# Performance work log

Hardware: AMD Instinct MI355X
Metric: run time of the kernel (lower is better)

Reference implementation:

```python
import jax, jax.numpy as jnp
import numpy as np

NUM_CLASSES = 21
EPS = 1e-6
MOMENTUM = 0.99
K_WEAK = 16
K_STRONG = 256
PROB_THRESH = 0.95
IGNORE = 255
NEG = -1e30


def _normalize(x, axis=-1):
    # matches F.normalize(p=2) / CosineSimilarity with eps=1e-6
    n = jnp.linalg.norm(x, axis=axis, keepdims=True)
    return x / jnp.maximum(n, EPS)


def setup_inputs() -> dict:
    key = jax.random.key(0)
    k0, k1, k2, k3, k4, k5 = jax.random.split(key, 6)
    B, C, H, W = 8, 256, 128, 128
    feature_weak = jax.random.normal(k0, (B, C, H, W), jnp.float32)
    feature_strong = jax.random.normal(k1, (B, C, H, W), jnp.float32)
    probablity_weak = jax.random.uniform(k2, (B, H, W), jnp.float32)
    memory_bank = jax.random.normal(k3, (NUM_CLASSES, 1, C), jnp.float32)
    pred_weak = jax.random.randint(k4, (B, H, W), 0, NUM_CLASSES)
    ignore_mask = jax.random.randint(k5, (B, H, W), 0, 256)
    return {
        'feature_weak': feature_weak,
        'feature_strong': feature_strong,
        'probablity_weak': probablity_weak,
        'memory_bank': memory_bank,
        'pred_weak': pred_weak,
        'ignore_mask': ignore_mask,
    }


def reference(feature_weak, feature_strong, probablity_weak, memory_bank, pred_weak, ignore_mask):
    B, C, H, W = feature_weak.shape
    N = B * H * W
    fw = feature_weak.transpose(0, 2, 3, 1).reshape(N, C)   # weak pixel feats
    fs = feature_strong.transpose(0, 2, 3, 1).reshape(N, C) # strong pixel feats
    seg = pred_weak.reshape(N)
    ign = ignore_mask.reshape(N)  # same-size bilinear resize (align_corners) is identity
    prob = probablity_weak.reshape(N)

    valid = ign != IGNORE
    conf = valid & (prob > PROB_THRESH)

    cls = jnp.arange(NUM_CLASSES)
    is_cls = seg[None, :] == cls[:, None]        # [K, N]
    m_weak = is_cls & conf[None, :]              # per-class high-confidence mask
    m_strong = is_cls & valid[None, :]
    n_weak = m_weak.sum(axis=1)                  # [K]
    n_strong = m_strong.sum(axis=1)

    protos = memory_bank[:, 0, :]                # [K, C]
    pn = _normalize(protos)
    sim_w = _normalize(fw) @ pn.T                # [N, K] cos(pixel_weak, proto)
    sim_s = _normalize(fs) @ pn.T                # [N, K] cos(pixel_strong, proto)

    sw = jnp.where(m_weak, sim_w.T, NEG)         # [K, N]
    ss = jnp.where(m_strong, -sim_s.T, NEG)      # negate -> bottom-k via top_k
    _, idx_w = jax.lax.top_k(sw, K_WEAK)         # [K, 16] most-similar weak pixels
    _, idx_s = jax.lax.top_k(ss, K_STRONG)       # [K, 256] least-similar strong pixels

    # select_feature duplicates the top element: slots are ranks [0,0,1,...,14]
    ranks = jnp.maximum(jnp.arange(K_WEAK) - 1, 0)
    sel_w = fw[idx_w[:, ranks]]                  # [K, 16, C]
    sel_s = fs[idx_s]                            # [K, 256, C]

    kw = jnp.minimum(K_WEAK, n_weak)
    ks = jnp.minimum(K_STRONG, n_strong)
    valid_w = jnp.arange(K_WEAK)[None, :] < kw[:, None]     # [K, 16]
    valid_s = jnp.arange(K_STRONG)[None, :] < ks[:, None]   # [K, 256]

    # calculate_loss: weak side detached, max over strong dim, sum / strong count
    wn = _normalize(jax.lax.stop_gradient(sel_w))
    sn = _normalize(sel_s)
    cosm = jnp.einsum('kwc,ksc->kws', wn, sn)    # [K, 16, 256]
    cosm = jnp.where(valid_s[:, None, :], cosm, NEG)
    max_sim = jnp.where(valid_w, cosm.max(axis=2), 0.0)     # [K, 16]
    class_ok = (n_weak > 0) & (n_strong > 0)
    sim_sum = jnp.where(class_ok, max_sim.sum(axis=1), 0.0).sum()
    count = jnp.where(class_ok, ks, 0).sum()
    loss = jnp.where(count > 0, 1.0 - sim_sum / count, 0.0)

    # update_memory: per-class mean of high-confidence weak feats, EMA scatter
    fw_ng = jax.lax.stop_gradient(fw)            # .data copy -> no grad
    wsum = m_weak.astype(fw.dtype) @ fw_ng       # [K, C] segmented sum
    mean = wsum / jnp.maximum(n_weak, 1).astype(fw.dtype)[:, None]
    new_protos = jnp.where((n_weak > 0)[:, None],
                           MOMENTUM * protos + (1.0 - MOMENTUM) * mean,
                           protos)
    new_memory_bank = new_protos[:, None, :]     # [K, 1, C]
    return loss, new_memory_bank
```

## Files before the change

kernel.cpp:

```cpp
#include <hip/hip_runtime.h>
#include <stdint.h>

#define NCLS  21
#define CDIM  256
#define HWSZ  16384
#define NPIX  131072
#define EPSV  1e-6f
#define NEGV  -1e30f
#define CAP_W 4096
#define CAP_S 16384
#define KSEL  256
#define NCC   8
#define CCH   (CDIM/NCC)
#define NPART 8
#define NBLK2 (NPIX/512)
#define WPAR  8

__device__ __forceinline__ uint64_t pack_key(float v, unsigned idx) {
  unsigned u = __float_as_uint(v);
  u = (u & 0x80000000u) ? ~u : (u | 0x80000000u);
  return ((uint64_t)(~u) << 32) | (uint64_t)idx;
}

__global__ void k0_init(const float* __restrict__ mb, float* pn, float* wsum) {
  int k = blockIdx.x, t = threadIdx.x;
  float v = mb[k * CDIM + t];
  float s = v * v;
  for (int o = 32; o > 0; o >>= 1) s += __shfl_down(s, o, 64);
  __shared__ float wsh[4];
  int wid = t >> 6, lane = t & 63;
  if (lane == 0) wsh[wid] = s;
  __syncthreads();
  float tot = wsh[0] + wsh[1] + wsh[2] + wsh[3];
  float inv = 1.0f / fmaxf(sqrtf(tot), EPSV);
  pn[k * CDIM + t] = v * inv;
  wsum[k * CDIM + t] = 0.0f;
}

__global__ void k1a_stream(const float* __restrict__ fw, const float* __restrict__ fs,
                           const float* __restrict__ prob, const int* __restrict__ seg,
                           const int* __restrict__ ign, const float* __restrict__ pn,
                           float* part, int* cnts) {
  __shared__ float pnT[CCH * NCLS];
  __shared__ int hs[NCLS], hw2[NCLS];
  int t = threadIdx.x;
  int pg = blockIdx.x;
  int cc = blockIdx.y;
  int c0 = cc * CCH;
  for (int i = t; i < CCH * NCLS; i += 256) {
    int c = i / NCLS, k = i % NCLS;
    pnT[i] = pn[k * CDIM + c0 + c];
  }
  if (cc == 0) {
    for (int i = t; i < NCLS; i += 256) { hs[i] = 0; hw2[i] = 0; }
  }
  __syncthreads();

  int n0 = pg * 512 + t * 2;
  int b = n0 >> 14, hw = n0 & (HWSZ - 1);
  int2   sg = *(const int2*)(seg + n0);
  int2   ig = *(const int2*)(ign + n0);
  float2 pr = *(const float2*)(prob + n0);
  if (cc == 0) {
    bool v0 = (ig.x != 255), v1 = (ig.y != 255);
    if (v0) atomicAdd(&hs[sg.x], 1);
    if (v1) atomicAdd(&hs[sg.y], 1);
    if (v0 && pr.x > 0.95f) atomicAdd(&hw2[sg.x], 1);
    if (v1 && pr.y > 0.95f) atomicAdd(&hw2[sg.y], 1);
  }

  const float* fwp = fw + ((size_t)b * CDIM + c0) * HWSZ + hw;
  const float* fsp = fs + ((size_t)b * CDIM + c0) * HWSZ + hw;

  float2 dw = {0,0}, nw = {0,0}, dsv = {0,0}, ns = {0,0};
#pragma unroll 8
  for (int cl = 0; cl < CCH; ++cl) {
    float2 a = *(const float2*)(fwp + (size_t)cl * HWSZ);
    float2 s = *(const float2*)(fsp + (size_t)cl * HWSZ);
    float p0 = pnT[cl * NCLS + sg.x];
    float p1 = pnT[cl * NCLS + sg.y];
    dw.x = fmaf(a.x, p0, dw.x); nw.x = fmaf(a.x, a.x, nw.x);
    dw.y = fmaf(a.y, p1, dw.y); nw.y = fmaf(a.y, a.y, nw.y);
    dsv.x = fmaf(s.x, p0, dsv.x); ns.x = fmaf(s.x, s.x, ns.x);
    dsv.y = fmaf(s.y, p1, dsv.y); ns.y = fmaf(s.y, s.y, ns.y);
  }
  float4* pp = (float4*)part + ((size_t)cc * NPIX + n0);
  pp[0] = make_float4(dw.x, nw.x, dsv.x, ns.x);
  pp[1] = make_float4(dw.y, nw.y, dsv.y, ns.y);

  if (cc == 0) {
    __syncthreads();
    for (int i = t; i < NCLS; i += 256) {
      cnts[pg * NCLS + i] = hs[i];
      cnts[NBLK2 * NCLS + pg * NCLS + i] = hw2[i];
    }
  }
}

__global__ void ks_scan(const int* __restrict__ cnts, int* offs, int* scnt, int* wcnt) {
  __shared__ int L[2 * NBLK2 * NCLS];
  int t = threadIdx.x;
  for (int i = t; i < 2 * NBLK2 * NCLS; i += 256) L[i] = cnts[i];
  __syncthreads();
  if (t < 2 * NCLS) {
    int q = t % NCLS;
    int typ = t / NCLS;
    int base = typ * NBLK2 * NCLS;
    int run = 0;
    for (int b2 = 0; b2 < NBLK2; ++b2) {
      int v = L[base + b2 * NCLS + q];
      L[base + b2 * NCLS + q] = run;
      run += v;
    }
    if (typ == 0) scnt[q] = run; else wcnt[q] = run;
  }
  __syncthreads();
  for (int i = t; i < 2 * NBLK2 * NCLS; i += 256) offs[i] = L[i];
}

__global__ void k1b_write(const float* __restrict__ part, const float* __restrict__ prob,
                          const int* __restrict__ seg, const int* __restrict__ ign,
                          const int* __restrict__ offs, uint64_t* wkeys, uint64_t* skeys) {
  __shared__ int ls[NCLS], lw[NCLS];
  int t = threadIdx.x, pg = blockIdx.x;
  if (t < NCLS) {
    ls[t] = offs[pg * NCLS + t];
    lw[t] = offs[NBLK2 * NCLS + pg * NCLS + t];
  }
  __syncthreads();
  int n0 = pg * 512 + t * 2;
  int2   sg = *(const int2*)(seg + n0);
  int2   ig = *(const int2*)(ign + n0);
  float2 pr = *(const float2*)(prob + n0);
  float dw[2] = {0,0}, nw[2] = {0,0}, ds[2] = {0,0}, ns[2] = {0,0};
#pragma unroll
  for (int cc = 0; cc < NCC; ++cc) {
    const float4* pp = (const float4*)part + ((size_t)cc * NPIX + n0);
#pragma unroll
    for (int i = 0; i < 2; ++i) {
      float4 v = pp[i];
      dw[i] += v.x; nw[i] += v.y; ds[i] += v.z; ns[i] += v.w;
    }
  }
  int   sga[2] = {sg.x, sg.y};
  int   iga[2] = {ig.x, ig.y};
  float pra[2] = {pr.x, pr.y};
#pragma unroll
  for (int i = 0; i < 2; ++i) {
    if (iga[i] != 255) {
      int q = sga[i];
      float sim_s = ds[i] / fmaxf(sqrtf(ns[i]), EPSV);
      int pos = atomicAdd(&ls[q], 1);
      if (pos < CAP_S) skeys[(size_t)q * CAP_S + pos] = pack_key(-sim_s, (unsigned)(n0 + i));
      if (pra[i] > 0.95f) {
        float sim_w = dw[i] / fmaxf(sqrtf(nw[i]), EPSV);
        int pw = atomicAdd(&lw[q], 1);
        if (pw < CAP_W) wkeys[(size_t)q * CAP_W + pw] = pack_key(sim_w, (unsigned)(n0 + i));
      }
    }
  }
}

__global__ void kw_sum(const float* __restrict__ fw, const uint64_t* __restrict__ wkeys,
                       const int* __restrict__ wcnt, float* wsum) {
  int k = blockIdx.x, p = blockIdx.y, t = threadIdx.x;
  int cnt = min(wcnt[k], CAP_W);
  float acc = 0.0f;
  for (int i = p; i < cnt; i += WPAR) {
    unsigned idx = (unsigned)(wkeys[(size_t)k * CAP_W + i] & 0xFFFFFFFFull);
    int b = idx >> 14, hw = idx & (HWSZ - 1);
    acc += fw[((size_t)(b * CDIM) + t) * HWSZ + hw];
  }
  if (acc != 0.0f) atomicAdd(&wsum[k * CDIM + t], acc);
}

__device__ void select_topk(const uint64_t* __restrict__ list, int cnt,
                            uint64_t* T, uint64_t* P, int* pcnt, int* woff) {
  int t = threadIdx.x;
  T[t] = ~0ull;
  if (t == 0) *pcnt = 0;
  __syncthreads();
  for (int base = 0; base < cnt; base += 256) {
    uint64_t key = (base + t < cnt) ? list[base + t] : ~0ull;
    uint64_t cutoff = T[KSEL - 1];
    bool pred = key < cutoff;
    unsigned long long mask = __ballot(pred);
    int wid = t >> 6, lane = t & 63;
    if (lane == 0) woff[wid] = __popcll(mask);
    int prefix = __popcll(mask & ((1ull << lane) - 1ull));
    __syncthreads();
    int off = 0;
    for (int w2 = 0; w2 < wid; ++w2) off += woff[w2];
    int total = woff[0] + woff[1] + woff[2] + woff[3];
    int old = *pcnt;
    if (pred) P[old + off + prefix] = key;
    int newc = old + total;
    __syncthreads();
    if (t == 0) *pcnt = newc;
    bool last = (base + 256 >= cnt);
    if (newc >= KSEL || (last && newc > 0)) {
      for (int i2 = t; i2 < 2 * KSEL; i2 += 256)
        if (i2 >= newc) P[i2] = ~0ull;
      for (unsigned size = 2; size <= 2 * KSEL; size <<= 1) {
        for (unsigned stride = size >> 1; stride > 0; stride >>= 1) {
          __syncthreads();
          unsigned lo = stride - 1;
          unsigned i = (((unsigned)t & ~lo) << 1) | ((unsigned)t & lo);
          unsigned j = i | stride;
          uint64_t a = P[i], b = P[j];
          bool up = ((i & size) == 0);
          if ((a > b) == up) { P[i] = b; P[j] = a; }
        }
      }
      __syncthreads();
      uint64_t a = T[t], b = P[KSEL - 1 - t];
      T[t] = a < b ? a : b;
      for (unsigned stride = KSEL / 2; stride > 0; stride >>= 1) {
        __syncthreads();
        if (((unsigned)t & stride) == 0) {
          uint64_t x = T[t], y = T[t + stride];
          if (x > y) { T[t] = y; T[t + stride] = x; }
        }
      }
      __syncthreads();
      if (t == 0) *pcnt = 0;
      __syncthreads();
    } else {
      __syncthreads();
    }
  }
}

__global__ void k2_topk(const uint64_t* __restrict__ wkeys, const uint64_t* __restrict__ skeys,
                        const int* wcnt, const int* scnt,
                        uint64_t* psel, int* idxw, int* kwv, int* nwv) {
  __shared__ uint64_t T[KSEL];
  __shared__ uint64_t P[2 * KSEL];
  __shared__ int pcnt;
  __shared__ int woff[4];
  int bid = blockIdx.x, t = threadIdx.x;
  if (bid < NCLS * NPART) {
    int k = bid / NPART, p = bid % NPART;
    int cnt = min(scnt[k], CAP_S);
    int chunk = (cnt + NPART - 1) / NPART;
    int lo = p * chunk;
    int hi = min(lo + chunk, cnt);
    int c = hi > lo ? hi - lo : 0;
    select_topk(skeys + (size_t)k * CAP_S + lo, c, T, P, &pcnt, woff);
    psel[((size_t)k * NPART + p) * KSEL + t] = T[t];
  } else {
    int k = bid - NCLS * NPART;
    int cnt_total = wcnt[k];
    int cnt = min(cnt_total, CAP_W);
    select_topk(wkeys + (size_t)k * CAP_W, cnt, T, P, &pcnt, woff);
    if (t < 16) idxw[k * 16 + t] = (int)(unsigned)(T[t] & 0xFFFFFFFFull);
    if (t == 0) { nwv[k] = cnt_total; kwv[k] = min(cnt_total, 16); }
  }
}

__global__ void k2m_merge(const uint64_t* __restrict__ psel, const int* scnt,
                          int* idxs, int* ksv, int* nsv) {
  int k = blockIdx.x, t = threadIdx.x;
  __shared__ uint64_t M[NPART * KSEL];
  for (int i = t; i < NPART * KSEL; i += 256) M[i] = psel[(size_t)k * NPART * KSEL + i];
  for (unsigned size = 2; size <= NPART * KSEL; size <<= 1) {
    for (unsigned stride = size >> 1; stride > 0; stride >>= 1) {
      __syncthreads();
      for (unsigned q = t; q < NPART * KSEL / 2; q += 256) {
        unsigned lo = stride - 1;
        unsigned i = ((q & ~lo) << 1) | (q & lo);
        unsigned j = i | stride;
        uint64_t a = M[i], b = M[j];
        bool up = ((i & size) == 0);
        if ((a > b) == up) { M[i] = b; M[j] = a; }
      }
    }
  }
  __syncthreads();
  idxs[k * KSEL + t] = (int)(unsigned)(M[t] & 0xFFFFFFFFull);
  if (t == 0) { int c = scnt[k]; nsv[k] = c; ksv[k] = c < KSEL ? c : KSEL; }
}

__global__ void k3a_gather(const float* __restrict__ fw, const float* __restrict__ fs,
                           const int* __restrict__ idxw, const int* __restrict__ idxs,
                           const int* __restrict__ kwv, const int* __restrict__ ksv,
                           float* dw_dense, float* ds_dense) {
  int k = blockIdx.y;
  int s0 = blockIdx.x * 4;
  int t = threadIdx.x;
  int wid = t >> 6, lane = t & 63;
  float v[4];
  bool strong[4];
  int slot_[4];
#pragma unroll
  for (int j = 0; j < 4; ++j) {
    int slot = s0 + j;
    slot_[j] = slot;
    strong[j] = slot < KSEL;
    bool ok;
    int n = 0;
    if (strong[j]) {
      ok = slot < ksv[k];
      if (ok) n = idxs[k * KSEL + slot];
    } else {
      int i = slot - KSEL;
      ok = i < kwv[k];
      int rank = i > 0 ? i - 1 : 0;
      if (ok) n = idxw[k * 16 + rank];
    }
    v[j] = 0.0f;
    if (ok) {
      int b = n >> 14, hw = n & (HWSZ - 1);
      const float* f = strong[j] ? fs : fw;
      v[j] = f[(size_t)(b * CDIM + t) * HWSZ + hw];
    }
  }
  __shared__ float wsh[4][4];
  float s[4];
#pragma unroll
  for (int j = 0; j < 4; ++j) {
    s[j] = v[j] * v[j];
    for (int o = 32; o > 0; o >>= 1) s[j] += __shfl_down(s[j], o, 64);
  }
  if (lane == 0) {
#pragma unroll
    for (int j = 0; j < 4; ++j) wsh[wid][j] = s[j];
  }
  __syncthreads();
#pragma unroll
  for (int j = 0; j < 4; ++j) {
    float tot = wsh[0][j] + wsh[1][j] + wsh[2][j] + wsh[3][j];
    float inv = 1.0f / fmaxf(sqrtf(tot), EPSV);
    float out = v[j] * inv;
    if (strong[j]) ds_dense[((size_t)k * KSEL + slot_[j]) * CDIM + t] = out;
    else           dw_dense[((size_t)k * 16 + (slot_[j] - KSEL)) * CDIM + t] = out;
  }
}

__global__ void k3b_loss(const float* __restrict__ dw_dense, const float* __restrict__ ds_dense,
                         const int* kwv, const int* ksv, const int* nwv, const int* nsv,
                         float* simsum, int* countk) {
  int k = blockIdx.x, t = threadIdx.x;
  int wid = t >> 6, lane = t & 63;
  __shared__ float wn[16 * CDIM];
  __shared__ float wred[4][16];
  for (int i = t; i < 16 * CDIM; i += 256) wn[i] = dw_dense[(size_t)k * 16 * CDIM + i];
  __syncthreads();
  int ks_ = ksv[k], kw_ = kwv[k];
  bool ok = (nwv[k] > 0) && (nsv[k] > 0);
  float dots[16];
#pragma unroll
  for (int i = 0; i < 16; ++i) dots[i] = 0.0f;
  bool jv = ok && (t < ks_);
  if (jv) {
    const float4* sp = (const float4*)(ds_dense + ((size_t)k * KSEL + t) * CDIM);
    for (int c4 = 0; c4 < CDIM / 4; ++c4) {
      float4 v = sp[c4];
#pragma unroll
      for (int i = 0; i < 16; ++i) {
        float4 w = ((const float4*)(wn + i * CDIM))[c4];
        dots[i] = fmaf(v.x, w.x, dots[i]);
        dots[i] = fmaf(v.y, w.y, dots[i]);
        dots[i] = fmaf(v.z, w.z, dots[i]);
        dots[i] = fmaf(v.w, w.w, dots[i]);
      }
    }
  }
#pragma unroll
  for (int i = 0; i < 16; ++i) {
    float v = jv ? dots[i] : NEGV;
    for (int o = 32; o > 0; o >>= 1) v = fmaxf(v, __shfl_down(v, o, 64));
    if (lane == 0) wred[wid][i] = v;
  }
  __syncthreads();
  if (t == 0) {
    float csum = 0.0f;
    for (int i = 0; i < kw_; ++i) {
      float m = fmaxf(fmaxf(wred[0][i], wred[1][i]), fmaxf(wred[2][i], wred[3][i]));
      csum += m;
    }
    simsum[k] = ok ? csum : 0.0f;
    countk[k] = ok ? ks_ : 0;
  }
}

__global__ void k4_final(const float* __restrict__ mb, const float* __restrict__ wsum,
                         const int* __restrict__ nwv, const float* __restrict__ simsum,
                         const int* __restrict__ countk, float* out) {
  int k = blockIdx.x, t = threadIdx.x;
  float p = mb[k * CDIM + t];
  float o = p;
  int nw = nwv[k];
  if (nw > 0) {
    float mean = wsum[k * CDIM + t] / (float)nw;
    o = 0.99f * p + 0.01f * mean;
  }
  out[1 + k * CDIM + t] = o;
  if (k == 0 && t == 0) {
    float ss = 0.0f;
    int cc = 0;
    for (int q = 0; q < NCLS; ++q) { ss += simsum[q]; cc += countk[q]; }
    out[0] = (cc > 0) ? (1.0f - ss / (float)cc) : 0.0f;
  }
}

extern "C" void kernel_launch(void* const* d_in, const int* in_sizes, int n_in,
                              void* d_out, int out_size, void* d_ws, size_t ws_size,
                              hipStream_t stream) {
  const float* fw   = (const float*)d_in[0];
  const float* fs   = (const float*)d_in[1];
  const float* prob = (const float*)d_in[2];
  const float* mb   = (const float*)d_in[3];
  const int*   seg  = (const int*)d_in[4];
  const int*   ign  = (const int*)d_in[5];
  float* out = (float*)d_out;

  char* ws = (char*)d_ws;
  size_t off = 0;
  auto alloc = [&](size_t bytes) -> char* {
    char* p = ws + off;
    off = (off + bytes + 255) & ~(size_t)255;
    return p;
  };
  float*    pn       = (float*)alloc(NCLS * CDIM * 4);
  float*    wsum     = (float*)alloc(NCLS * CDIM * 4);
  int*      wcnt     = (int*)alloc(NCLS * 4);
  int*      scnt     = (int*)alloc(NCLS * 4);
  int*      idxw     = (int*)alloc(NCLS * 16 * 4);
  int*      idxs     = (int*)alloc(NCLS * KSEL * 4);
  int*      kwv      = (int*)alloc(NCLS * 4);
  int*      ksv      = (int*)alloc(NCLS * 4);
  int*      nwv      = (int*)alloc(NCLS * 4);
  int*      nsv      = (int*)alloc(NCLS * 4);
  float*    simsum   = (float*)alloc(NCLS * 4);
  int*      countk   = (int*)alloc(NCLS * 4);
  int*      cnts     = (int*)alloc(2 * NBLK2 * NCLS * 4);
  int*      offs     = (int*)alloc(2 * NBLK2 * NCLS * 4);
  uint64_t* wkeys    = (uint64_t*)alloc((size_t)NCLS * CAP_W * 8);
  uint64_t* skeys    = (uint64_t*)alloc((size_t)NCLS * CAP_S * 8);
  uint64_t* psel     = (uint64_t*)alloc((size_t)NCLS * NPART * KSEL * 8);
  float*    dw_dense = (float*)alloc((size_t)NCLS * 16 * CDIM * 4);
  float*    ds_dense = (float*)alloc((size_t)NCLS * KSEL * CDIM * 4);
  float*    part     = (float*)alloc((size_t)NCC * NPIX * 4 * 4);
  (void)in_sizes; (void)n_in; (void)out_size; (void)ws_size;

  k0_init<<<NCLS, 256, 0, stream>>>(mb, pn, wsum);
  k1a_stream<<<dim3(NBLK2, NCC), 256, 0, stream>>>(fw, fs, prob, seg, ign, pn,
                                                   part, cnts);
  ks_scan<<<1, 256, 0, stream>>>(cnts, offs, scnt, wcnt);
  k1b_write<<<NBLK2, 256, 0, stream>>>(part, prob, seg, ign, offs, wkeys, skeys);
  kw_sum<<<dim3(NCLS, WPAR), 256, 0, stream>>>(fw, wkeys, wcnt, wsum);
  k2_topk<<<NCLS * NPART + NCLS, 256, 0, stream>>>(wkeys, skeys, wcnt, scnt,
                                                   psel, idxw, kwv, nwv);
  k2m_merge<<<NCLS, 256, 0, stream>>>(psel, scnt, idxs, ksv, nsv);
  k3a_gather<<<dim3((KSEL + 16) / 4, NCLS), 256, 0, stream>>>(fw, fs, idxw, idxs, kwv, ksv,
                                                              dw_dense, ds_dense);
  k3b_loss<<<NCLS, 256, 0, stream>>>(dw_dense, ds_dense, kwv, ksv, nwv, nsv,
                                     simsum, countk);
  k4_final<<<NCLS, 256, 0, stream>>>(mb, wsum, nwv, simsum, countk, out);
}
```

Measured before the change: 460.0 us.

## Fuse weak-feature class sums into streaming pass and use bitonic min-merge for top-k

```diff
diff --git a/kernel.cpp b/kernel.cpp
--- a/kernel.cpp
+++ b/kernel.cpp
@@ -14,7 +14,8 @@
 #define CCH   (CDIM/NCC)
 #define NPART 8
 #define NBLK2 (NPIX/512)
-#define WPAR  8
+#define P2    2048
+#define NPG   (NPIX/P2)
 
 __device__ __forceinline__ uint64_t pack_key(float v, unsigned idx) {
   unsigned u = __float_as_uint(v);
@@ -37,12 +38,13 @@
   wsum[k * CDIM + t] = 0.0f;
 }
 
-__global__ void k1a_stream(const float* __restrict__ fw, const float* __restrict__ fs,
-                           const float* __restrict__ prob, const int* __restrict__ seg,
-                           const int* __restrict__ ign, const float* __restrict__ pn,
-                           float* part, int* cnts) {
+__global__ __launch_bounds__(256, 2)
+void k1a_stream(const float* __restrict__ fw, const float* __restrict__ fs,
+                const float* __restrict__ prob, const int* __restrict__ seg,
+                const int* __restrict__ ign, const float* __restrict__ pn,
+                float* part, float* wsum) {
   __shared__ float pnT[CCH * NCLS];
-  __shared__ int hs[NCLS], hw2[NCLS];
+  __shared__ float wloc[NCLS * (CCH + 1)];
   int t = threadIdx.x;
   int pg = blockIdx.x;
   int cc = blockIdx.y;
@@ -51,49 +53,79 @@
     int c = i / NCLS, k = i % NCLS;
     pnT[i] = pn[k * CDIM + c0 + c];
   }
-  if (cc == 0) {
-    for (int i = t; i < NCLS; i += 256) { hs[i] = 0; hw2[i] = 0; }
-  }
-  __syncthreads();
-
+  for (int i = t; i < NCLS * (CCH + 1); i += 256) wloc[i] = 0.0f;
+  __syncthreads();
+
+  int base = pg * P2;
+  int b = base >> 14;
+  int hwb = (base & (HWSZ - 1)) + t;
+
+  int sgv[8]; bool cf[8];
+  float dw[8], nw[8], dsv[8], nsv[8];
+#pragma unroll
+  for (int i = 0; i < 8; ++i) {
+    int px = base + i * 256 + t;
+    sgv[i] = seg[px];
+    int igv = ign[px];
+    float prv = prob[px];
+    cf[i] = (igv != 255) && (prv > 0.95f);
+    dw[i] = nw[i] = dsv[i] = nsv[i] = 0.0f;
+  }
+
+  const float* fwp = fw + ((size_t)b * CDIM + c0) * HWSZ + hwb;
+  const float* fsp = fs + ((size_t)b * CDIM + c0) * HWSZ + hwb;
+
+#pragma unroll 4
+  for (int c = 0; c < CCH; ++c) {
+    size_t co = (size_t)c * HWSZ;
+    float a[8], s8[8];
+#pragma unroll
+    for (int i = 0; i < 8; ++i) a[i] = fwp[co + i * 256];
+#pragma unroll
+    for (int i = 0; i < 8; ++i) s8[i] = fsp[co + i * 256];
+#pragma unroll
+    for (int i = 0; i < 8; ++i) {
+      float p = pnT[c * NCLS + sgv[i]];
+      dw[i]  = fmaf(a[i],  p,     dw[i]);
+      nw[i]  = fmaf(a[i],  a[i],  nw[i]);
+      dsv[i] = fmaf(s8[i], p,     dsv[i]);
+      nsv[i] = fmaf(s8[i], s8[i], nsv[i]);
+      if (cf[i]) atomicAdd(&wloc[sgv[i] * (CCH + 1) + c], a[i]);
+    }
+  }
+
+  float4* pp = (float4*)part + (size_t)cc * NPIX + base + t;
+#pragma unroll
+  for (int i = 0; i < 8; ++i)
+    pp[i * 256] = make_float4(dw[i], nw[i], dsv[i], nsv[i]);
+
+  __syncthreads();
+  for (int i = t; i < NCLS * CCH; i += 256) {
+    int k = i / CCH, cl = i % CCH;
+    float v = wloc[k * (CCH + 1) + cl];
+    if (v != 0.0f) atomicAdd(&wsum[k * CDIM + c0 + cl], v);
+  }
+}
+
+__global__ void k1c_count(const float* __restrict__ prob, const int* __restrict__ seg,
+                          const int* __restrict__ ign, int* cnts) {
+  __shared__ int hs[NCLS], hw2[NCLS];
+  int t = threadIdx.x, pg = blockIdx.x;
+  for (int i = t; i < NCLS; i += 256) { hs[i] = 0; hw2[i] = 0; }
+  __syncthreads();
   int n0 = pg * 512 + t * 2;
-  int b = n0 >> 14, hw = n0 & (HWSZ - 1);
   int2   sg = *(const int2*)(seg + n0);
   int2   ig = *(const int2*)(ign + n0);
   float2 pr = *(const float2*)(prob + n0);
-  if (cc == 0) {
-    bool v0 = (ig.x != 255), v1 = (ig.y != 255);
-    if (v0) atomicAdd(&hs[sg.x], 1);
-    if (v1) atomicAdd(&hs[sg.y], 1);
-    if (v0 && pr.x > 0.95f) atomicAdd(&hw2[sg.x], 1);
-    if (v1 && pr.y > 0.95f) atomicAdd(&hw2[sg.y], 1);
-  }
-
-  const float* fwp = fw + ((size_t)b * CDIM + c0) * HWSZ + hw;
-  const float* fsp = fs + ((size_t)b * CDIM + c0) * HWSZ + hw;
-
-  float2 dw = {0,0}, nw = {0,0}, dsv = {0,0}, ns = {0,0};
-#pragma unroll 8
-  for (int cl = 0; cl < CCH; ++cl) {
-    float2 a = *(const float2*)(fwp + (size_t)cl * HWSZ);
-    float2 s = *(const float2*)(fsp + (size_t)cl * HWSZ);
-    float p0 = pnT[cl * NCLS + sg.x];
-    float p1 = pnT[cl * NCLS + sg.y];
-    dw.x = fmaf(a.x, p0, dw.x); nw.x = fmaf(a.x, a.x, nw.x);
-    dw.y = fmaf(a.y, p1, dw.y); nw.y = fmaf(a.y, a.y, nw.y);
-    dsv.x = fmaf(s.x, p0, dsv.x); ns.x = fmaf(s.x, s.x, ns.x);
-    dsv.y = fmaf(s.y, p1, dsv.y); ns.y = fmaf(s.y, s.y, ns.y);
-  }
-  float4* pp = (float4*)part + ((size_t)cc * NPIX + n0);
-  pp[0] = make_float4(dw.x, nw.x, dsv.x, ns.x);
-  pp[1] = make_float4(dw.y, nw.y, dsv.y, ns.y);
-
-  if (cc == 0) {
-    __syncthreads();
-    for (int i = t; i < NCLS; i += 256) {
-      cnts[pg * NCLS + i] = hs[i];
-      cnts[NBLK2 * NCLS + pg * NCLS + i] = hw2[i];
-    }
+  bool v0 = (ig.x != 255), v1 = (ig.y != 255);
+  if (v0) atomicAdd(&hs[sg.x], 1);
+  if (v1) atomicAdd(&hs[sg.y], 1);
+  if (v0 && pr.x > 0.95f) atomicAdd(&hw2[sg.x], 1);
+  if (v1 && pr.y > 0.95f) atomicAdd(&hw2[sg.y], 1);
+  __syncthreads();
+  for (int i = t; i < NCLS; i += 256) {
+    cnts[pg * NCLS + i] = hs[i];
+    cnts[NBLK2 * NCLS + pg * NCLS + i] = hw2[i];
   }
 }
 
@@ -159,19 +191,6 @@
       }
     }
   }
-}
-
-__global__ void kw_sum(const float* __restrict__ fw, const uint64_t* __restrict__ wkeys,
-                       const int* __restrict__ wcnt, float* wsum) {
-  int k = blockIdx.x, p = blockIdx.y, t = threadIdx.x;
-  int cnt = min(wcnt[k], CAP_W);
-  float acc = 0.0f;
-  for (int i = p; i < cnt; i += WPAR) {
-    unsigned idx = (unsigned)(wkeys[(size_t)k * CAP_W + i] & 0xFFFFFFFFull);
-    int b = idx >> 14, hw = idx & (HWSZ - 1);
-    acc += fw[((size_t)(b * CDIM) + t) * HWSZ + hw];
-  }
-  if (acc != 0.0f) atomicAdd(&wsum[k * CDIM + t], acc);
 }
 
 __device__ void select_topk(const uint64_t* __restrict__ list, int cnt,
@@ -262,22 +281,57 @@
                           int* idxs, int* ksv, int* nsv) {
   int k = blockIdx.x, t = threadIdx.x;
   __shared__ uint64_t M[NPART * KSEL];
+  __shared__ uint64_t M2[4 * KSEL];
   for (int i = t; i < NPART * KSEL; i += 256) M[i] = psel[(size_t)k * NPART * KSEL + i];
-  for (unsigned size = 2; size <= NPART * KSEL; size <<= 1) {
-    for (unsigned stride = size >> 1; stride > 0; stride >>= 1) {
-      __syncthreads();
-      for (unsigned q = t; q < NPART * KSEL / 2; q += 256) {
-        unsigned lo = stride - 1;
-        unsigned i = ((q & ~lo) << 1) | (q & lo);
-        unsigned j = i | stride;
-        uint64_t a = M[i], b = M[j];
-        bool up = ((i & size) == 0);
-        if ((a > b) == up) { M[i] = b; M[j] = a; }
-      }
-    }
-  }
-  __syncthreads();
-  idxs[k * KSEL + t] = (int)(unsigned)(M[t] & 0xFFFFFFFFull);
+  __syncthreads();
+#pragma unroll
+  for (int p = 0; p < 4; ++p) {
+    uint64_t a = M[p * 512 + t], b = M[p * 512 + 511 - t];
+    M2[p * 256 + t] = a < b ? a : b;
+  }
+  for (int str = 128; str > 0; str >>= 1) {
+    __syncthreads();
+    for (int q = t; q < 4 * 128; q += 256) {
+      int list = q >> 7, r = q & 127;
+      int i = ((r & ~(str - 1)) << 1) | (r & (str - 1));
+      int ai = list * 256 + i, bi = ai + str;
+      uint64_t x = M2[ai], y = M2[bi];
+      if (x > y) { M2[ai] = y; M2[bi] = x; }
+    }
+  }
+  __syncthreads();
+#pragma unroll
+  for (int p = 0; p < 2; ++p) {
+    uint64_t a = M2[p * 512 + t], b = M2[p * 512 + 511 - t];
+    M[p * 256 + t] = a < b ? a : b;
+  }
+  for (int str = 128; str > 0; str >>= 1) {
+    __syncthreads();
+    {
+      int q = t;
+      int list = q >> 7, r = q & 127;
+      int i = ((r & ~(str - 1)) << 1) | (r & (str - 1));
+      int ai = list * 256 + i, bi = ai + str;
+      uint64_t x = M[ai], y = M[bi];
+      if (x > y) { M[ai] = y; M[bi] = x; }
+    }
+  }
+  __syncthreads();
+  {
+    uint64_t a = M[t], b = M[511 - t];
+    M2[t] = a < b ? a : b;
+  }
+  for (int str = 128; str > 0; str >>= 1) {
+    __syncthreads();
+    if (t < 128) {
+      int r = t;
+      int i = ((r & ~(str - 1)) << 1) | (r & (str - 1));
+      uint64_t x = M2[i], y = M2[i + str];
+      if (x > y) { M2[i] = y; M2[i + str] = x; }
+    }
+  }
+  __syncthreads();
+  idxs[k * KSEL + t] = (int)(unsigned)(M2[t] & 0xFFFFFFFFull);
   if (t == 0) { int c = scnt[k]; nsv[k] = c; ksv[k] = c < KSEL ? c : KSEL; }
 }
 
@@ -445,11 +499,11 @@
   (void)in_sizes; (void)n_in; (void)out_size; (void)ws_size;
 
   k0_init<<<NCLS, 256, 0, stream>>>(mb, pn, wsum);
-  k1a_stream<<<dim3(NBLK2, NCC), 256, 0, stream>>>(fw, fs, prob, seg, ign, pn,
-                                                   part, cnts);
+  k1a_stream<<<dim3(NPG, NCC), 256, 0, stream>>>(fw, fs, prob, seg, ign, pn,
+                                                 part, wsum);
+  k1c_count<<<NBLK2, 256, 0, stream>>>(prob, seg, ign, cnts);
   ks_scan<<<1, 256, 0, stream>>>(cnts, offs, scnt, wcnt);
   k1b_write<<<NBLK2, 256, 0, stream>>>(part, prob, seg, ign, offs, wkeys, skeys);
-  kw_sum<<<dim3(NCLS, WPAR), 256, 0, stream>>>(fw, wkeys, wcnt, wsum);
   k2_topk<<<NCLS * NPART + NCLS, 256, 0, stream>>>(wkeys, skeys, wcnt, scnt,
                                                    psel, idxw, kwv, nwv);
   k2m_merge<<<NCLS, 256, 0, stream>>>(psel, scnt, idxs, ksv, nsv);
```

New measurement: 403.1 us. 1.14x faster.
